# Kernel tuning notes

Measured on AMD Instinct MI355X. Metric: run time of the kernel, lower is better.

The kernel has to match this reference:

```python
import jax, jax.numpy as jnp
import numpy as np

B, HIST, PRED, CITY, FEAT, HID = 512, 8, 24, 184, 13, 32


def setup_inputs() -> dict:
    key = jax.random.key(0)
    ks = jax.random.split(key, 10)
    s = 0.1
    return {
        "pm25_hist": jax.random.normal(ks[0], (B, HIST, CITY, 1), jnp.float32),
        "feature": jax.random.normal(ks[1], (B, HIST + PRED, CITY, FEAT), jnp.float32),
        "W_in": jax.random.normal(ks[2], (HID, FEAT + 1), jnp.float32) * s,
        "b_in": jax.random.normal(ks[3], (HID,), jnp.float32) * s,
        "W_out": jax.random.normal(ks[4], (1, HID), jnp.float32) * s,
        "b_out": jax.random.normal(ks[5], (1,), jnp.float32) * s,
        "W_ih": jax.random.normal(ks[6], (4 * HID, HID), jnp.float32) * s,
        "W_hh": jax.random.normal(ks[7], (4 * HID, HID), jnp.float32) * s,
        "b_ih": jax.random.normal(ks[8], (4 * HID,), jnp.float32) * s,
        "b_hh": jax.random.normal(ks[9], (4 * HID,), jnp.float32) * s,
    }


def reference(pm25_hist, feature, W_in, b_in, W_out, b_out, W_ih, W_hh, b_ih, b_hh):
    BC = B * CITY
    # future features, time-major: [PRED, B*CITY, FEAT]
    feat_fut = feature[:, HIST:HIST + PRED]              # [B, PRED, CITY, FEAT]
    feat_fut = jnp.transpose(feat_fut, (1, 0, 2, 3)).reshape(PRED, BC, FEAT)

    h0 = jnp.zeros((BC, HID), pm25_hist.dtype)
    c0 = jnp.zeros((BC, HID), pm25_hist.dtype)
    x0 = pm25_hist[:, -1].reshape(BC, 1)                 # last observed pm25

    def step(carry, feat_t):
        hn, cn, xn = carry
        x = jnp.concatenate([xn, feat_t], axis=-1)        # [BC, in_dim]
        x = x @ W_in.T + b_in                             # fc_in -> [BC, HID]
        gates = x @ W_ih.T + b_ih + hn @ W_hh.T + b_hh    # [BC, 4*HID]
        i, f, g, o = jnp.split(gates, 4, axis=-1)
        i, f, o = jax.nn.sigmoid(i), jax.nn.sigmoid(f), jax.nn.sigmoid(o)
        g = jnp.tanh(g)
        cn = f * cn + i * g
        hn = o * jnp.tanh(cn)
        xn = hn @ W_out.T + b_out                         # fc_out -> [BC, 1]
        return (hn, cn, xn), xn

    _, ys = jax.lax.scan(step, (h0, c0, x0), feat_fut)    # ys: [PRED, BC, 1]
    ys = ys.reshape(PRED, B, CITY, 1)
    return jnp.transpose(ys, (1, 0, 2, 3))                # [B, PRED, CITY, 1]
```

## Files before the change

### kernel.cpp

```cpp
#include <hip/hip_runtime.h>
#include <hip/hip_bf16.h>

#define B_    512
#define HIST_ 8
#define PRED_ 24
#define CITY_ 184
#define FEAT_ 13
#define HID_  32
#define BC_   (B_*CITY_)
#define FLAG_OFF 7168


struct TrueT  { static constexpr bool value = true;  };
struct FalseT { static constexpr bool value = false; };

typedef _Float16 v8hf __attribute__((ext_vector_type(8)));
typedef _Float16 v4hf __attribute__((ext_vector_type(4)));
typedef float    v4f  __attribute__((ext_vector_type(4)));

__device__ __forceinline__ float rcp_(float x) { return __builtin_amdgcn_rcpf(x); }
__device__ __forceinline__ float sigf(float x) { return rcp_(1.0f + __expf(-x)); }
__device__ __forceinline__ float tanhf_(float x) {
    float e = __expf(2.0f * x);
    return 1.0f - 2.0f * rcp_(e + 1.0f);
}

template<bool F32>
__device__ __forceinline__ float ldin(const void* p, long i) {
    if constexpr (F32) return ((const float*)p)[i];
    else               return __bfloat162float(((const __hip_bfloat16*)p)[i]);
}
template<bool F32>
__device__ __forceinline__ void stout(void* p, long i, float v) {
    if constexpr (F32) ((float*)p)[i] = v;
    else               ((__hip_bfloat16*)p)[i] = __float2bfloat16(v);
}

__device__ __forceinline__ v4f mfma_k32(v8hf a, v8hf b, v4f c) {
    return __builtin_amdgcn_mfma_f32_16x16x32_f16(a, b, c, 0, 0, 0);
}
__device__ __forceinline__ v4f mfma_k16(v4hf a, v4hf b, v4f c) {
#if __has_builtin(__builtin_amdgcn_mfma_f32_16x16x16f16)
    return __builtin_amdgcn_mfma_f32_16x16x16f16(a, b, c, 0, 0, 0);
#else
    v8hf a8; v8hf b8;
    #pragma unroll
    for (int j = 0; j < 4; ++j) { a8[j] = a[j]; b8[j] = b[j]; }
    #pragma unroll
    for (int j = 4; j < 8; ++j) { a8[j] = (_Float16)0.f; b8[j] = (_Float16)0.f; }
    return __builtin_amdgcn_mfma_f32_16x16x32_f16(a8, b8, c, 0, 0, 0);
#endif
}

template<bool F32>
__device__ __forceinline__ void prep_body(const void* W_in, const void* b_in,
                                          const void* W_out, const void* b_out,
                                          const void* W_ih, const void* W_hh,
                                          const void* b_ih, const void* b_hh,
                                          float* ws, int j)
{
    if (j >= 128) return;
    const int gate = j >> 5;
    const int u    = j & 31;
    const int qb   = u >> 3;
    const int psi  = u & 7;
    const int tt   = 2*gate + (psi >> 2);
    const int p    = 16*tt + 4*qb + (psi & 3);

    float wx[14];
    #pragma unroll
    for (int c = 0; c < 14; ++c) wx[c] = 0.0f;
    float bg = ldin<F32>(b_ih, j) + ldin<F32>(b_hh, j);
    #pragma unroll
    for (int m = 0; m < 32; ++m) {
        float wihm = ldin<F32>(W_ih, j*32 + m);
        #pragma unroll
        for (int c = 0; c < 14; ++c) wx[c] = fmaf(wihm, ldin<F32>(W_in, m*14 + c), wx[c]);
        bg = fmaf(wihm, ldin<F32>(b_in, m), bg);
    }
    float a0 = wx[0];
    #pragma unroll
    for (int k = 0; k < 32; ++k)
        ws[p*32 + k] = ldin<F32>(W_hh, j*32 + k) + a0 * ldin<F32>(W_out, k);
    #pragma unroll
    for (int f = 0; f < 13; ++f) ws[4096 + p*16 + f] = wx[1 + f];
    #pragma unroll
    for (int f = 13; f < 16; ++f) ws[4096 + p*16 + f] = 0.0f;
    float bo = ldin<F32>(b_out, 0);
    ws[6144 + p] = bg + a0 * bo;
    ws[6272 + p] = a0;
    ws[6400 + p] = bg;
    if (j < 32) ws[6528 + j] = ldin<F32>(W_out, j);
    if (j == 0) ws[6560] = bo;
}

__global__ void prep_all(const unsigned short* __restrict__ feat_raw,
                         const void* __restrict__ W_in,  const void* __restrict__ b_in,
                         const void* __restrict__ W_out, const void* __restrict__ b_out,
                         const void* __restrict__ W_ih,  const void* __restrict__ W_hh,
                         const void* __restrict__ b_ih,  const void* __restrict__ b_hh,
                         float* __restrict__ ws)
{
    __shared__ int cnt;
    const int tid = threadIdx.x;
    if (tid == 0) cnt = 0;
    __syncthreads();
    int insane = 0;
    for (int i = tid; i < 4096; i += 128) {
        float v = __uint_as_float(((unsigned int)feat_raw[i]) << 16);
        if (!(fabsf(v) < 1e8f)) insane++;
    }
    if (insane) atomicAdd(&cnt, insane);
    __syncthreads();
    const bool f32 = (cnt > 8);
    if (tid == 0) ws[FLAG_OFF] = f32 ? 1.0f : 0.0f;
    if (f32) prep_body<true >(W_in,b_in,W_out,b_out,W_ih,W_hh,b_ih,b_hh,ws,tid);
    else     prep_body<false>(W_in,b_in,W_out,b_out,W_ih,W_hh,b_ih,b_hh,ws,tid);
}

template<bool F32>
__device__ __forceinline__ void lstm_body(const void* __restrict__ pm25,
                                          const void* __restrict__ feat,
                                          const float* __restrict__ ws,
                                          void* __restrict__ out)
{
    const int lane = threadIdx.x & 63;
    const int rho  = lane & 15;
    const int q    = lane >> 4;
    const int wv   = threadIdx.x >> 6;
    const int wseq = (blockIdx.x*4 + wv) * 16;
    const int seq  = wseq + rho;
    const int bb   = seq / CITY_;
    const int city = seq - bb*CITY_;

    v8hf Whi0[8], Wlo0[8];
    v4hf Whi1[8], Wlo1[8];
    v4f  bias2[8];
    #pragma unroll
    for (int tt = 0; tt < 8; ++tt) {
        const float* wr = ws + (16*tt + rho)*32 + 8*q;
        #pragma unroll
        for (int j = 0; j < 8; ++j) {
            const float w = wr[j];
            const _Float16 h = (_Float16)w;
            Whi0[tt][j] = h;
            Wlo0[tt][j] = (_Float16)(w - (float)h);
        }
        const float* wf = ws + 4096 + (16*tt + rho)*16 + 4*q;
        #pragma unroll
        for (int j = 0; j < 4; ++j) {
            const float w = wf[j];
            const _Float16 h = (_Float16)w;
            Whi1[tt][j] = h;
            Wlo1[tt][j] = (_Float16)(w - (float)h);
        }
        bias2[tt] = *(const v4f*)(ws + 6144 + 16*tt + 4*q);
    }
    float wo8[8];
    #pragma unroll
    for (int j = 0; j < 8; ++j) wo8[j] = ws[6528 + 8*q + j];
    const float bo = ws[6560];
    const long obase = (long)bb*PRED_*CITY_ + city;

    int eoff[4];
    #pragma unroll
    for (int j = 0; j < 4; ++j) {
        const int e = 4*q + j;
        eoff[j] = (e < FEAT_) ? e : (FEAT_-1);
    }
    long fbase = ((long)(bb*(HIST_+PRED_) + HIST_)*CITY_ + city)*FEAT_;
    float fn[4];
    auto ldfeat = [&]() {
        #pragma unroll
        for (int j = 0; j < 4; ++j) fn[j] = ldin<F32>(feat, fbase + eoff[j]);
        fbase += CITY_ * FEAT_;
    };
    v4hf fhi, flo;
    auto convf = [&]() {
        #pragma unroll
        for (int j = 0; j < 4; ++j) {
            const _Float16 fh = (_Float16)fn[j];
            fhi[j] = fh;
            if constexpr (F32) flo[j] = (_Float16)(fn[j] - (float)fh);
        }
    };

    float cst[8];
    v8hf  xhi, xlo;

    auto finishT = [&](v4f (&acc)[8], int t, auto T0flag) {
        constexpr bool T0 = decltype(T0flag)::value;
        float h[8];
        #pragma unroll
        for (int psi = 0; psi < 8; ++psi) {
            const int tl = psi >> 2, r = psi & 3;
            const float I = sigf(acc[tl][r]);
            const float G = tanhf_(acc[4+tl][r]);
            const float O = sigf(acc[6+tl][r]);
            float c;
            if constexpr (T0) c = I*G;
            else              c = fmaf(sigf(acc[2+tl][r]), cst[psi], I*G);
            cst[psi] = c;
            h[psi] = O * tanhf_(c);
        }
        #pragma unroll
        for (int psi = 0; psi < 8; ++psi) {
            const _Float16 hh = (_Float16)h[psi];
            xhi[psi] = hh;
            xlo[psi] = (_Float16)(h[psi] - (float)hh);
        }
        float y = 0.0f;
        #pragma unroll
        for (int psi = 0; psi < 8; ++psi) y = fmaf(wo8[psi], h[psi], y);
        y += __shfl_xor(y, 16);
        y += __shfl_xor(y, 32);
        if (q == 0) stout<F32>(out, obase + (long)t*CITY_, y + bo);
    };

    ldfeat();
    convf();
    ldfeat();
    {
        const float x0 = ldin<F32>(pm25, (long)(bb*HIST_ + (HIST_-1))*CITY_ + city);
        v4f acc[8];
        #pragma unroll
        for (int tt = 0; tt < 8; ++tt) {
            const v4f bg0 = *(const v4f*)(ws + 6400 + 16*tt + 4*q);
            const v4f a0  = *(const v4f*)(ws + 6272 + 16*tt + 4*q);
            v4f c;
            #pragma unroll
            for (int r = 0; r < 4; ++r) c[r] = fmaf(a0[r], x0, bg0[r]);
            v4f a = mfma_k16(Whi1[tt], fhi, c);
            a = mfma_k16(Wlo1[tt], fhi, a);
            if constexpr (F32) a = mfma_k16(Whi1[tt], flo, a);
            acc[tt] = a;
        }
        finishT(acc, 0, TrueT{});
    }

    #pragma unroll 1
    for (int t = 1; t < PRED_; ++t) {
        convf();
        if (t < PRED_-1) ldfeat();
        v4f acc[8];
        #pragma unroll
        for (int tt = 0; tt < 8; ++tt) {
            v4f a = mfma_k32(Whi0[tt], xhi, bias2[tt]);
            a = mfma_k32(Wlo0[tt], xhi, a);
            a = mfma_k32(Whi0[tt], xlo, a);
            a = mfma_k16(Whi1[tt], fhi, a);
            a = mfma_k16(Wlo1[tt], fhi, a);
            if constexpr (F32) a = mfma_k16(Whi1[tt], flo, a);
            acc[tt] = a;
        }
        finishT(acc, t, FalseT{});
    }
}

__global__ __launch_bounds__(256, 2) void lstm_main(
    const void* __restrict__ pm25,
    const void* __restrict__ feat,
    const float* __restrict__ ws,
    void* __restrict__ out)
{
    const bool f32 = (ws[FLAG_OFF] == 1.0f);
    if (f32) lstm_body<true >(pm25, feat, ws, out);
    else     lstm_body<false>(pm25, feat, ws, out);
}

extern "C" void kernel_launch(void* const* d_in, const int* in_sizes, int n_in,
                              void* d_out, int out_size, void* d_ws, size_t ws_size,
                              hipStream_t stream) {
    const void* pm25  = d_in[0];
    const void* feat  = d_in[1];
    const void* W_in  = d_in[2];
    const void* b_in  = d_in[3];
    const void* W_out = d_in[4];
    const void* b_out = d_in[5];
    const void* W_ih  = d_in[6];
    const void* W_hh  = d_in[7];
    const void* b_ih  = d_in[8];
    const void* b_hh  = d_in[9];
    float* ws = (float*)d_ws;

    prep_all<<<dim3(1), dim3(128), 0, stream>>>(
        (const unsigned short*)feat, W_in, b_in, W_out, b_out,
        W_ih, W_hh, b_ih, b_hh, ws);

    lstm_main<<<dim3(BC_/64), dim3(256), 0, stream>>>(pm25, feat, ws, d_out);
}
```

Baseline: 359.5 us.

## Batch reciprocals in gate activations, use packed fp16 converts, single-wave blocks, setprio

Reworks the LSTM cell's nonlinearities so four reciprocals share one rcp instruction through product tricks. Inputs to exp are clamped to avoid overflow in that batched path. Uses packed round-toward-zero fp16 conversion for the hi/lo splits of h and the features. Launches one wave per block with a different launch bound, and raises wave priority around the MFMA chains to overlap with other waves' transcendental work. Risks include slightly changed rounding (RTZ vs RNE in the splits), reduced precision from the batched reciprocal, and register-pressure changes from the new launch bounds.

```diff
diff --git a/kernel.cpp b/kernel.cpp
--- a/kernel.cpp
+++ b/kernel.cpp
@@ -16,13 +16,23 @@
 
 typedef _Float16 v8hf __attribute__((ext_vector_type(8)));
 typedef _Float16 v4hf __attribute__((ext_vector_type(4)));
+typedef _Float16 v2hf __attribute__((ext_vector_type(2)));
 typedef float    v4f  __attribute__((ext_vector_type(4)));
 
+__device__ __forceinline__ v2hf pkrtz(float a, float b) {
+    return __builtin_bit_cast(v2hf, __builtin_amdgcn_cvt_pkrtz(a, b));
+}
+
 __device__ __forceinline__ float rcp_(float x) { return __builtin_amdgcn_rcpf(x); }
-__device__ __forceinline__ float sigf(float x) { return rcp_(1.0f + __expf(-x)); }
-__device__ __forceinline__ float tanhf_(float x) {
-    float e = __expf(2.0f * x);
-    return 1.0f - 2.0f * rcp_(e + 1.0f);
+__device__ __forceinline__ float cl20(float x) { return fminf(fmaxf(x, -20.0f), 20.0f); }
+
+__device__ __forceinline__ void inv4(float a, float b, float c, float d,
+                                     float& ia, float& ib, float& ic, float& id)
+{
+    const float ab = a*b, cd = c*d;
+    const float r  = rcp_(ab*cd);
+    const float iab = r*cd, icd = r*ab;
+    ia = iab*b; ib = iab*a; ic = icd*d; id = icd*c;
 }
 
 template<bool F32>
@@ -127,8 +137,7 @@
     const int lane = threadIdx.x & 63;
     const int rho  = lane & 15;
     const int q    = lane >> 4;
-    const int wv   = threadIdx.x >> 6;
-    const int wseq = (blockIdx.x*4 + wv) * 16;
+    const int wseq = blockIdx.x * 16;
     const int seq  = wseq + rho;
     const int bb   = seq / CITY_;
     const int city = seq - bb*CITY_;
@@ -178,10 +187,14 @@
     v4hf fhi, flo;
     auto convf = [&]() {
         #pragma unroll
-        for (int j = 0; j < 4; ++j) {
-            const _Float16 fh = (_Float16)fn[j];
-            fhi[j] = fh;
-            if constexpr (F32) flo[j] = (_Float16)(fn[j] - (float)fh);
+        for (int jj = 0; jj < 2; ++jj) {
+            const v2hf ph = pkrtz(fn[2*jj], fn[2*jj+1]);
+            fhi[2*jj] = ph[0]; fhi[2*jj+1] = ph[1];
+            if constexpr (F32) {
+                const v2hf pl = pkrtz(fn[2*jj] - (float)ph[0],
+                                      fn[2*jj+1] - (float)ph[1]);
+                flo[2*jj] = pl[0]; flo[2*jj+1] = pl[1];
+            }
         }
     };
 
@@ -191,27 +204,50 @@
     auto finishT = [&](v4f (&acc)[8], int t, auto T0flag) {
         constexpr bool T0 = decltype(T0flag)::value;
         float h[8];
-        #pragma unroll
-        for (int psi = 0; psi < 8; ++psi) {
-            const int tl = psi >> 2, r = psi & 3;
-            const float I = sigf(acc[tl][r]);
-            const float G = tanhf_(acc[4+tl][r]);
-            const float O = sigf(acc[6+tl][r]);
-            float c;
-            if constexpr (T0) c = I*G;
-            else              c = fmaf(sigf(acc[2+tl][r]), cst[psi], I*G);
-            cst[psi] = c;
-            h[psi] = O * tanhf_(c);
-        }
-        #pragma unroll
-        for (int psi = 0; psi < 8; ++psi) {
-            const _Float16 hh = (_Float16)h[psi];
-            xhi[psi] = hh;
-            xlo[psi] = (_Float16)(h[psi] - (float)hh);
-        }
         float y = 0.0f;
         #pragma unroll
-        for (int psi = 0; psi < 8; ++psi) y = fmaf(wo8[psi], h[psi], y);
+        for (int hf = 0; hf < 2; ++hf) {
+            float di[4], df[4], dg[4], dq[4];
+            #pragma unroll
+            for (int r = 0; r < 4; ++r) {
+                di[r] = 1.0f + __expf(-cl20(acc[hf    ][r]));
+                df[r] = 1.0f + __expf(-cl20(acc[2 + hf][r]));
+                dg[r] = 1.0f + __expf( cl20(acc[4 + hf][r] * 2.0f));
+                dq[r] = 1.0f + __expf(-cl20(acc[6 + hf][r]));
+            }
+            float I[4], F[4], Gi[4], O[4];
+            inv4(di[0],di[1],di[2],di[3], I[0],I[1],I[2],I[3]);
+            inv4(df[0],df[1],df[2],df[3], F[0],F[1],F[2],F[3]);
+            inv4(dg[0],dg[1],dg[2],dg[3], Gi[0],Gi[1],Gi[2],Gi[3]);
+            inv4(dq[0],dq[1],dq[2],dq[3], O[0],O[1],O[2],O[3]);
+            float dc[4];
+            #pragma unroll
+            for (int r = 0; r < 4; ++r) {
+                const float G  = 1.0f - 2.0f*Gi[r];
+                const float ig = I[r]*G;
+                float c;
+                if constexpr (T0) c = ig;
+                else              c = fmaf(F[r], cst[4*hf + r], ig);
+                cst[4*hf + r] = c;
+                dc[r] = 1.0f + __expf(cl20(c * 2.0f));
+            }
+            float Tc[4];
+            inv4(dc[0],dc[1],dc[2],dc[3], Tc[0],Tc[1],Tc[2],Tc[3]);
+            #pragma unroll
+            for (int r = 0; r < 4; ++r) {
+                const float hv = O[r] * (1.0f - 2.0f*Tc[r]);
+                h[4*hf + r] = hv;
+                y = fmaf(wo8[4*hf + r], hv, y);
+            }
+        }
+        #pragma unroll
+        for (int jj = 0; jj < 4; ++jj) {
+            const v2hf ph = pkrtz(h[2*jj], h[2*jj+1]);
+            xhi[2*jj] = ph[0]; xhi[2*jj+1] = ph[1];
+            const v2hf pl = pkrtz(h[2*jj] - (float)ph[0],
+                                  h[2*jj+1] - (float)ph[1]);
+            xlo[2*jj] = pl[0]; xlo[2*jj+1] = pl[1];
+        }
         y += __shfl_xor(y, 16);
         y += __shfl_xor(y, 32);
         if (q == 0) stout<F32>(out, obase + (long)t*CITY_, y + bo);
@@ -223,6 +259,7 @@
     {
         const float x0 = ldin<F32>(pm25, (long)(bb*HIST_ + (HIST_-1))*CITY_ + city);
         v4f acc[8];
+        __builtin_amdgcn_s_setprio(1);
         #pragma unroll
         for (int tt = 0; tt < 8; ++tt) {
             const v4f bg0 = *(const v4f*)(ws + 6400 + 16*tt + 4*q);
@@ -235,6 +272,7 @@
             if constexpr (F32) a = mfma_k16(Whi1[tt], flo, a);
             acc[tt] = a;
         }
+        __builtin_amdgcn_s_setprio(0);
         finishT(acc, 0, TrueT{});
     }
 
@@ -243,6 +281,7 @@
         convf();
         if (t < PRED_-1) ldfeat();
         v4f acc[8];
+        __builtin_amdgcn_s_setprio(1);
         #pragma unroll
         for (int tt = 0; tt < 8; ++tt) {
             v4f a = mfma_k32(Whi0[tt], xhi, bias2[tt]);
@@ -253,11 +292,12 @@
             if constexpr (F32) a = mfma_k16(Whi1[tt], flo, a);
             acc[tt] = a;
         }
+        __builtin_amdgcn_s_setprio(0);
         finishT(acc, t, FalseT{});
     }
 }
 
-__global__ __launch_bounds__(256, 2) void lstm_main(
+__global__ __launch_bounds__(64, 4) void lstm_main(
     const void* __restrict__ pm25,
     const void* __restrict__ feat,
     const float* __restrict__ ws,
@@ -287,5 +327,5 @@
         (const unsigned short*)feat, W_in, b_in, W_out, b_out,
         W_ih, W_hh, b_ih, b_hh, ws);
 
-    lstm_main<<<dim3(BC_/64), dim3(256), 0, stream>>>(pm25, feat, ws, d_out);
-}
+    lstm_main<<<dim3(BC_/16), dim3(64), 0, stream>>>(pm25, feat, ws, d_out);
+}
```

Result: slower. 854.5 us (+137.7%).
